# Kernel optimization log

Hardware: AMD Instinct MI355X
Metric: run time of the kernel (lower is better)

The kernel has to match this reference:

```python
import jax, jax.numpy as jnp
import numpy as np

TEMPERATURE = 0.07
HARD_K = 10
N, D, NUM_CLASSES = 8192, 256, 128


def setup_inputs() -> dict:
    key = jax.random.key(0)
    kf, kl = jax.random.split(key)
    feats = jax.random.normal(kf, (N, D), dtype=jnp.float32)
    labels = jax.random.randint(kl, (N,), 0, NUM_CLASSES, dtype=jnp.int64)
    return {"feats": feats, "labels": labels}


def _loss(feats, labels):
    n = feats.shape[0]
    # F.normalize(dim=-1) with eps=1e-12
    norm = jnp.maximum(jnp.linalg.norm(feats, axis=-1, keepdims=True), 1e-12)
    z = feats / norm
    sim = (z @ z.T) / TEMPERATURE  # [N, N]

    same = labels[:, None] == labels[None, :]
    eye = jnp.eye(n, dtype=bool)
    same_ns = same & ~eye          # same label, excluding self
    diff = ~same                   # different label

    neg_inf = jnp.float32(-jnp.inf)
    # uniform random positive per row via Gumbel-max over the same-label mask
    g = jax.random.gumbel(jax.random.key(42), (n, n), dtype=jnp.float32)
    pos_idx = jnp.argmax(jnp.where(same_ns, g, neg_inf), axis=1)  # [N]
    pos_logit = jnp.take_along_axis(sim, pos_idx[:, None], axis=1)[:, 0]

    # hard negatives: top-k of sims over different-label columns
    neg_sims = jnp.where(diff, sim, neg_inf)
    hard_vals, _ = jax.lax.top_k(neg_sims, HARD_K)  # [N, K]; exp(-inf)=0 handles rows with <K negatives

    num = jnp.exp(pos_logit)
    den = num + jnp.sum(jnp.exp(hard_vals), axis=1)
    li = -jnp.log(jnp.maximum(num / jnp.maximum(den, 1e-8), 1e-8))

    valid = jnp.any(same_ns, axis=1) & jnp.any(diff, axis=1)
    cnt = jnp.maximum(jnp.sum(valid), 1)
    return jnp.sum(jnp.where(valid, li, 0.0)) / cnt.astype(li.dtype)


def reference(feats, labels):
    return _loss(feats, labels)
```

## Files before the change

### kernel.cpp

```cpp
#include <hip/hip_runtime.h>
#include <cstdint>
#include <math.h>

#define N_     8192
#define D_     256
#define NLBL   128
#define TEMP_INV 14.285714285714286f
#define HARDK  10
#define THETA  0.16f
#define GCAP   256

#define NCHUNK 32
#define CHUNK  (N_ / NCHUNK)
#define TILES  (CHUNK / 32)
#define CSLOT  16

typedef __attribute__((ext_vector_type(8)))  short bf16x8;
typedef __attribute__((ext_vector_type(16))) float f32x16;

__device__ __forceinline__ uint32_t rotl32(uint32_t x, int n) {
  return (x << n) | (x >> (32 - n));
}
__device__ uint32_t tf_bits(uint32_t idx) {
  uint32_t x0 = 0u, x1 = idx;
  const uint32_t k0 = 0u, k1 = 42u;
  const uint32_t k2 = k0 ^ k1 ^ 0x1BD11BDAu;
  x0 += k0; x1 += k1;
#define TFR(r) { x0 += x1; x1 = rotl32(x1, r); x1 ^= x0; }
  TFR(13) TFR(15) TFR(26) TFR(6)
  x0 += k1; x1 += k2 + 1u;
  TFR(17) TFR(29) TFR(16) TFR(24)
  x0 += k2; x1 += k0 + 2u;
  TFR(13) TFR(15) TFR(26) TFR(6)
  x0 += k0; x1 += k1 + 3u;
  TFR(17) TFR(29) TFR(16) TFR(24)
  x0 += k1; x1 += k2 + 4u;
  TFR(13) TFR(15) TFR(26) TFR(6)
  x0 += k2; x1 += k0 + 5u;
#undef TFR
  return x0 ^ x1;
}

__device__ __forceinline__ uint32_t f2bf(float x) {
  uint32_t b = __float_as_uint(x);
  return (b + 0x7FFFu + ((b >> 16) & 1u)) >> 16;
}

__global__ __launch_bounds__(256) void prep_group_kernel(
    const float* __restrict__ feats, const int* __restrict__ labels,
    float* __restrict__ inv_norm, unsigned short* __restrict__ zt,
    uint32_t* __restrict__ mask_g, int* __restrict__ glist, int* __restrict__ cnt_g) {
  __shared__ uint4 tile[16][33];
  __shared__ int lcnt;
  const int tid = threadIdx.x;

  if (blockIdx.x < 512) {
    const int row0 = blockIdx.x * 16;
    const int wv = tid >> 6, l = tid & 63;
#pragma unroll
    for (int rr = 0; rr < 4; ++rr) {
      const int rloc = wv * 4 + rr;
      const int row = row0 + rloc;
      float4 v = ((const float4*)feats)[(size_t)row * 64 + l];
      float ss = v.x * v.x + v.y * v.y + v.z * v.z + v.w * v.w;
#pragma unroll
      for (int o = 32; o; o >>= 1) ss += __shfl_xor(ss, o);
      float inv = 1.0f / fmaxf(sqrtf(ss), 1e-12f);
      if (l == 0) inv_norm[row] = inv;
      uint2 p;
      p.x = f2bf(v.x * inv) | (f2bf(v.y * inv) << 16);
      p.y = f2bf(v.z * inv) | (f2bf(v.w * inv) << 16);
      *(uint2*)((char*)&tile[0][0] + rloc * 528 + l * 8) = p;
    }
    __syncthreads();
#pragma unroll
    for (int it = 0; it < 2; ++it) {
      int idx = it * 256 + tid;
      int c = idx >> 4, r = idx & 15;
      ((uint4*)zt)[(size_t)c * N_ + row0 + r] = tile[r][c];
    }
  } else {
    const int b = blockIdx.x - 512;
    const int lane = tid & 63, wv = tid >> 6;
    if (tid == 0) lcnt = 0;
    __syncthreads();
    for (int it = 0; it < N_; it += 256) {
      int col = it + tid;
      bool pred = (labels[col] == b);
      unsigned long long m = __ballot(pred);
      if (lane == 0) {
        int w0 = (it + wv * 64) >> 5;
        mask_g[b * 256 + w0]     = (uint32_t)m;
        mask_g[b * 256 + w0 + 1] = (uint32_t)(m >> 32);
      }
      if (pred) {
        int p = atomicAdd(&lcnt, 1);
        if (p < GCAP) glist[b * GCAP + p] = col;
      }
    }
    __syncthreads();
    if (tid == 0) cnt_g[b] = lcnt;
  }
}

__device__ __forceinline__ void stage_tile(const unsigned short* zt, char (*AbK)[1024],
                                           int colT, int wid, int l, int kg) {
  const char* base = (const char*)zt + ((size_t)kg * N_ + colT + (l & 31)) * 16;
#pragma unroll
  for (int q = 0; q < 2; ++q) {
    const int kk = wid * 2 + q;
    __builtin_amdgcn_global_load_lds(
        (const __attribute__((address_space(1))) void*)(base + (size_t)kk * (2 * N_ * 16)),
        (__attribute__((address_space(3))) void*)(&AbK[kk][0]), 16, 0, 0);
  }
}

#define INS8(H0,H1,H2,H3,H4,H5,H6,H7,POS,C) \
  { H0 = (POS==0)?(C):H0; H1 = (POS==1)?(C):H1; H2 = (POS==2)?(C):H2; H3 = (POS==3)?(C):H3; \
    H4 = (POS==4)?(C):H4; H5 = (POS==5)?(C):H5; H6 = (POS==6)?(C):H6; H7 = (POS==7)?(C):H7; \
    ++POS; }

__global__ __launch_bounds__(512) void collect_kernel(const unsigned short* __restrict__ zt,
                                                      const int* __restrict__ labels,
                                                      const uint32_t* __restrict__ mask_g,
                                                      float* __restrict__ vals,
                                                      int* __restrict__ counts) {
  __shared__ char Ab[2][16][1024];

  const int tid = threadIdx.x;
  const int l = tid & 63, wid = tid >> 6;
  const int kg = l >> 5;
  const int bx = blockIdx.x;
  const int rc = bx & 31, cc = bx >> 5;
  const int row0 = rc * 256;
  const int col0 = cc * CHUNK;
  const int rowW = row0 + wid * 32 + (l & 31);
  const int lab = labels[rowW];

  uint32_t mW[TILES];
  {
    const uint4* mm = (const uint4*)(mask_g + lab * 256 + (col0 >> 5));
    uint4 m0 = mm[0], m1 = mm[1];
    mW[0]=m0.x; mW[1]=m0.y; mW[2]=m0.z; mW[3]=m0.w;
    mW[4]=m1.x; mW[5]=m1.y; mW[6]=m1.z; mW[7]=m1.w;
  }

  bf16x8 bf[16];
  {
    const uint4* ztq = (const uint4*)zt;
#pragma unroll
    for (int kk = 0; kk < 16; ++kk)
      bf[kk] = *(const bf16x8*)&ztq[(size_t)(kk * 2 + kg) * N_ + rowW];
  }

  float h0=0,h1=0,h2=0,h3=0,h4=0,h5=0,h6=0,h7=0;
  int pos = 0;
  float* vb = vals + ((size_t)rowW * NCHUNK + cc) * CSLOT + kg * 8;

  stage_tile(zt, Ab[0], col0, wid, l, kg);
  __syncthreads();

  int buf = 0;
#pragma unroll
  for (int t = 0; t < TILES; ++t) {
    if (t + 1 < TILES) stage_tile(zt, Ab[buf ^ 1], col0 + (t + 1) * 32, wid, l, kg);

    f32x16 acc;
#pragma unroll
    for (int r = 0; r < 16; ++r) acc[r] = 0.f;
    __builtin_amdgcn_s_setprio(1);
#pragma unroll
    for (int kk = 0; kk < 16; ++kk) {
      bf16x8 a = *(const bf16x8*)&Ab[buf][kk][l * 16];
      acc = __builtin_amdgcn_mfma_f32_32x32x16_bf16(a, bf[kk], acc, 0, 0, 0);
    }
    __builtin_amdgcn_s_setprio(0);

    const uint32_t wsh = mW[t] >> (kg * 4);
#pragma unroll
    for (int r = 0; r < 16; ++r) {
      const int cpos = (r & 3) + 8 * (r >> 2);
      bool hit = ((((wsh >> cpos) & 1u) == 0u) && (acc[r] > THETA));
      if (__any(hit)) {
        if (hit) { INS8(h0,h1,h2,h3,h4,h5,h6,h7, pos, acc[r]); }
      }
    }
    __syncthreads();
    buf ^= 1;
  }

  {
    float4 a0 = {h0, h1, h2, h3};
    float4 a1 = {h4, h5, h6, h7};
    *(float4*)(vb)     = a0;
    *(float4*)(vb + 4) = a1;
    counts[(rowW * NCHUNK + cc) * 2 + kg] = pos;
  }
}

__global__ __launch_bounds__(256) void finalize_kernel(
    const float* __restrict__ feats, const int* __restrict__ labels,
    const float* __restrict__ inv_norm,
    const int* __restrict__ glist, const int* __restrict__ cnt_g,
    const int* __restrict__ counts, const float* __restrict__ vals,
    float* __restrict__ li, int* __restrict__ valid) {
  const int row = blockIdx.x * 4 + (threadIdx.x >> 6);
  const int lane = threadIdx.x & 63;
  const int lab = labels[row];
  const int gc = cnt_g[lab];
  const int gn = gc < GCAP ? gc : GCAP;
  const float4* feats4 = (const float4*)feats;

  uint32_t bk = 0u; int bj = -1;
  for (int e = lane; e < gn; e += 64) {
    int j = glist[lab * GCAP + e];
    if (j != row) {
      uint32_t key = tf_bits((uint32_t)row * (uint32_t)N_ + (uint32_t)j) >> 9;
      if (bj < 0 || key > bk || (key == bk && j < bj)) { bk = key; bj = j; }
    }
  }
#pragma unroll
  for (int o = 32; o; o >>= 1) {
    uint32_t ok = __shfl_xor(bk, o);
    int oj = __shfl_xor(bj, o);
    if (oj >= 0 && (bj < 0 || ok > bk || (ok == bk && oj < bj))) { bk = ok; bj = oj; }
  }

  float pc = 0.f;
  if (bj >= 0) {
    float4 a = feats4[(size_t)row * 64 + lane];
    float4 b = feats4[(size_t)bj * 64 + lane];
    float p = a.x * b.x + a.y * b.y + a.z * b.z + a.w * b.w;
#pragma unroll
    for (int o = 32; o; o >>= 1) p += __shfl_xor(p, o);
    pc = p * inv_norm[row] * inv_norm[bj];
  }

  float vv[8];
  int ovf = 0;
#pragma unroll
  for (int q = 0; q < 8; ++q) {
    int s = lane + 64 * q;
    int cell = s >> 4, wi = s & 15;
    int c0 = counts[(row * NCHUNK + cell) * 2 + 0];
    int c1 = counts[(row * NCHUNK + cell) * 2 + 1];
    ovf |= ((c0 > 8) || (c1 > 8)) ? 1 : 0;
    float val = vals[(size_t)row * (NCHUNK * CSLOT) + s];
    bool live = (wi < 8) ? (wi < c0) : ((wi - 8) < c1);
    vv[q] = live ? val : -INFINITY;
  }

  float num = expf(pc * TEMP_INV);
  float den = num;
  int got = 0;
#pragma unroll 1
  for (int it = 0; it < HARDK; ++it) {
    float lm = fmaxf(fmaxf(fmaxf(vv[0], vv[1]), fmaxf(vv[2], vv[3])),
                     fmaxf(fmaxf(vv[4], vv[5]), fmaxf(vv[6], vv[7])));
    float wm = lm;
#pragma unroll
    for (int o = 32; o; o >>= 1) wm = fmaxf(wm, __shfl_xor(wm, o));
    if (wm < -1e37f) break;
    den += expf(wm * TEMP_INV);
    ++got;
    unsigned long long b = __ballot(lm == wm);
    int fl = __ffsll((long long)b) - 1;
    if (lane == fl) {
      if      (vv[0] == wm) vv[0] = -INFINITY;
      else if (vv[1] == wm) vv[1] = -INFINITY;
      else if (vv[2] == wm) vv[2] = -INFINITY;
      else if (vv[3] == wm) vv[3] = -INFINITY;
      else if (vv[4] == wm) vv[4] = -INFINITY;
      else if (vv[5] == wm) vv[5] = -INFINITY;
      else if (vv[6] == wm) vv[6] = -INFINITY;
      else                  vv[7] = -INFINITY;
    }
  }

  const int ndiff = N_ - gc;
  const bool vld = (bj >= 0) && (ndiff > 0);
  const int want = ndiff < HARDK ? ndiff : HARDK;

  if (vld && (__any(ovf) || got < want)) {
    float tk[HARDK];
#pragma unroll
    for (int k = 0; k < HARDK; ++k) tk[k] = -INFINITY;
    const float invr = inv_norm[row];
    const float4 a = feats4[(size_t)row * 64 + lane];
#pragma unroll 1
    for (int j = 0; j < N_; ++j) {
      if (j == row || labels[j] == lab) continue;
      float4 b = feats4[(size_t)j * 64 + lane];
      float p = a.x * b.x + a.y * b.y + a.z * b.z + a.w * b.w;
#pragma unroll
      for (int o = 32; o; o >>= 1) p += __shfl_xor(p, o);
      float c = p * invr * inv_norm[j];
      if (c > tk[0]) {
        tk[0] = c;
#pragma unroll
        for (int q = 0; q < HARDK - 1; ++q)
          if (tk[q] > tk[q + 1]) { float tmp = tk[q]; tk[q] = tk[q + 1]; tk[q + 1] = tmp; }
      }
    }
    den = num;
#pragma unroll
    for (int k = 0; k < HARDK; ++k)
      if (tk[k] > -1e37f) den += expf(tk[k] * TEMP_INV);
  }

  float L = 0.f;
  if (vld) L = -logf(fmaxf(num / fmaxf(den, 1e-8f), 1e-8f));
  if (lane == 0) {
    li[row] = L;
    valid[row] = vld ? 1 : 0;
  }
}

__global__ __launch_bounds__(256) void reduce_kernel(const float* __restrict__ li,
                                                     const int* __restrict__ valid,
                                                     float* __restrict__ out) {
  __shared__ float ssum[4];
  __shared__ int scnt[4];
  float s = 0.f; int c = 0;
  for (int i = threadIdx.x; i < N_; i += 256) { s += li[i]; c += valid[i]; }
#pragma unroll
  for (int o = 32; o; o >>= 1) { s += __shfl_down(s, o); c += __shfl_down(c, o); }
  if ((threadIdx.x & 63) == 0) { ssum[threadIdx.x >> 6] = s; scnt[threadIdx.x >> 6] = c; }
  __syncthreads();
  if (threadIdx.x == 0) {
    float S = 0.f; int C = 0;
    for (int w = 0; w < 4; ++w) { S += ssum[w]; C += scnt[w]; }
    out[0] = S / (float)(C > 0 ? C : 1);
  }
}

extern "C" void kernel_launch(void* const* d_in, const int* in_sizes, int n_in,
                              void* d_out, int out_size, void* d_ws, size_t ws_size,
                              hipStream_t stream) {
  const float* feats  = (const float*)d_in[0];
  const int*   labels = (const int*)d_in[1];
  float* out = (float*)d_out;

  char* w = (char*)d_ws;
  unsigned short* zt  = (unsigned short*)w;  w += (size_t)N_ * D_ * 2;
  float* inv_norm = (float*)w;               w += (size_t)N_ * 4;
  uint32_t* mask_g = (uint32_t*)w;           w += (size_t)NLBL * 256 * 4;
  int* glist = (int*)w;                      w += (size_t)NLBL * GCAP * 4;
  int* cnt_g = (int*)w;                      w += (size_t)NLBL * 4;
  int* counts = (int*)w;                     w += (size_t)N_ * NCHUNK * 2 * 4;
  float* vals = (float*)w;                   w += (size_t)N_ * NCHUNK * CSLOT * 4;
  float* li_arr = (float*)w;                 w += (size_t)N_ * 4;
  int* valid_arr = (int*)w;                  w += (size_t)N_ * 4;

  hipLaunchKernelGGL(prep_group_kernel, dim3(640), dim3(256), 0, stream,
                     feats, labels, inv_norm, zt, mask_g, glist, cnt_g);
  hipLaunchKernelGGL(collect_kernel, dim3(32 * NCHUNK), dim3(512), 0, stream,
                     zt, labels, mask_g, vals, counts);
  hipLaunchKernelGGL(finalize_kernel, dim3(N_ / 4), dim3(256), 0, stream,
                     feats, labels, inv_norm, glist, cnt_g, counts, vals, li_arr, valid_arr);
  hipLaunchKernelGGL(reduce_kernel, dim3(1), dim3(256), 0, stream, li_arr, valid_arr, out);
}
```

Baseline: 88.47 us.

## Exploit symmetry of similarity matrix by computing only upper-triangular tile blocks

The collect kernel now launches only the upper-triangular set of (row chunk, column chunk) blocks and, for off-diagonal blocks, also records the transposed hits into shared memory buffers that are then written to the mirrored rows' slots. This roughly halves the MFMA work for the N×N similarity. In exchange it adds LDS atomics and extra shared memory per block, a serial loop to decode the block index, and extra global writes. The transposed path depends on the mask being symmetric and on the per-cell hit cap of 8, and the half-slot assignment (mhalf from row bits) differs from the direct path's kg split, so overflow behaviour can diverge.

Measured after the change: 92.51 us. 1.05x slower.

```diff
diff --git a/kernel.cpp b/kernel.cpp
--- a/kernel.cpp
+++ b/kernel.cpp
@@ -126,16 +126,24 @@
                                                       float* __restrict__ vals,
                                                       int* __restrict__ counts) {
   __shared__ char Ab[2][16][1024];
+  __shared__ float mcell[256 * 2 * 8];
+  __shared__ int   mcnt[256 * 2];
 
   const int tid = threadIdx.x;
   const int l = tid & 63, wid = tid >> 6;
   const int kg = l >> 5;
-  const int bx = blockIdx.x;
-  const int rc = bx & 31, cc = bx >> 5;
+
+  int rc = 0, rem = blockIdx.x;
+  while (rem >= NCHUNK - rc) { rem -= NCHUNK - rc; ++rc; }
+  const int cc = rc + rem;
+  const bool offdiag = (cc > rc);
+
   const int row0 = rc * 256;
   const int col0 = cc * CHUNK;
   const int rowW = row0 + wid * 32 + (l & 31);
   const int lab = labels[rowW];
+
+  mcnt[tid] = 0;
 
   uint32_t mW[TILES];
   {
@@ -156,6 +164,7 @@
   float h0=0,h1=0,h2=0,h3=0,h4=0,h5=0,h6=0,h7=0;
   int pos = 0;
   float* vb = vals + ((size_t)rowW * NCHUNK + cc) * CSLOT + kg * 8;
+  const int mhalf = (rowW >> 2) & 1;
 
   stage_tile(zt, Ab[0], col0, wid, l, kg);
   __syncthreads();
@@ -182,7 +191,14 @@
       const int cpos = (r & 3) + 8 * (r >> 2);
       bool hit = ((((wsh >> cpos) & 1u) == 0u) && (acc[r] > THETA));
       if (__any(hit)) {
-        if (hit) { INS8(h0,h1,h2,h3,h4,h5,h6,h7, pos, acc[r]); }
+        if (hit) {
+          INS8(h0,h1,h2,h3,h4,h5,h6,h7, pos, acc[r]);
+          if (offdiag) {
+            int jc = t * 32 + cpos + 4 * kg;
+            int p = atomicAdd(&mcnt[jc * 2 + mhalf], 1);
+            if (p < 8) mcell[(jc * 2 + mhalf) * 8 + p] = acc[r];
+          }
+        }
       }
     }
     __syncthreads();
@@ -195,6 +211,17 @@
     *(float4*)(vb)     = a0;
     *(float4*)(vb + 4) = a1;
     counts[(rowW * NCHUNK + cc) * 2 + kg] = pos;
+  }
+
+  if (offdiag) {
+    int jc = tid >> 1, half = tid & 1;
+    int cnt = mcnt[jc * 2 + half];
+    float4 m0 = *(float4*)&mcell[(jc * 2 + half) * 8];
+    float4 m1 = *(float4*)&mcell[(jc * 2 + half) * 8 + 4];
+    float* dm = vals + ((size_t)(col0 + jc) * NCHUNK + rc) * CSLOT + half * 8;
+    *(float4*)(dm)     = m0;
+    *(float4*)(dm + 4) = m1;
+    counts[((col0 + jc) * NCHUNK + rc) * 2 + half] = cnt;
   }
 }
 
@@ -354,7 +381,7 @@
 
   hipLaunchKernelGGL(prep_group_kernel, dim3(640), dim3(256), 0, stream,
                      feats, labels, inv_norm, zt, mask_g, glist, cnt_g);
-  hipLaunchKernelGGL(collect_kernel, dim3(32 * NCHUNK), dim3(512), 0, stream,
+  hipLaunchKernelGGL(collect_kernel, dim3((NCHUNK * (NCHUNK + 1)) / 2), dim3(512), 0, stream,
                      zt, labels, mask_g, vals, counts);
   hipLaunchKernelGGL(finalize_kernel, dim3(N_ / 4), dim3(256), 0, stream,
                      feats, labels, inv_norm, glist, cnt_g, counts, vals, li_arr, valid_arr);
```
